# Kernel tuning notes

Measured on AMD Instinct MI355X. Metric: run time of the kernel, lower is better.

Reference implementation:

```python
import jax, jax.numpy as jnp
import numpy as np

N = 50000
E = 1600000
IN_F = 512
OUT_F = 128
NEG_SLOPE = 0.01   # nn.LeakyReLU() default
TEMPERATURE = 0.5


def setup_inputs() -> dict:
    key = jax.random.key(0)
    k1, k2, k3, k4 = jax.random.split(key, 4)
    h = jax.random.normal(k1, (N, IN_F), dtype=jnp.float32)
    # xavier_uniform with gain=1.414
    limW = 1.414 * np.sqrt(6.0 / (IN_F + OUT_F))
    W = jax.random.uniform(k2, (IN_F, OUT_F), minval=-limW, maxval=limW, dtype=jnp.float32)
    lima = 1.414 * np.sqrt(6.0 / (2 * OUT_F + 1))
    a = jax.random.uniform(k3, (2 * OUT_F, 1), minval=-lima, maxval=lima, dtype=jnp.float32)
    edge_index = jax.random.randint(k4, (2, E), 0, N, dtype=jnp.int64)
    return {"h": h, "W": W, "a": a, "edge_index": edge_index}


def reference(h, W, a, edge_index):
    # Inference: F.dropout(training=False) is identity.
    Wh = h @ W                                   # [N, F_out]
    src = edge_index[0]                          # row indices -> softmax segments
    dst = edge_index[1]
    # cat([Wh[src], Wh[dst]]) @ a == (Wh @ a1)[src] + (Wh @ a2)[dst]
    a1 = a[:OUT_F, 0]
    a2 = a[OUT_F:, 0]
    s1 = Wh @ a1                                 # [N]
    s2 = Wh @ a2                                 # [N]
    e = s1[src] + s2[dst]                        # [E]
    e = jnp.where(e >= 0, e, NEG_SLOPE * e)      # LeakyReLU
    logits = e / TEMPERATURE
    # sparse softmax over dim=1 (per source-node row segments)
    seg_max = jax.ops.segment_max(logits, src, num_segments=N)  # [N]
    ex = jnp.exp(logits - seg_max[src])          # [E]
    denom = jax.ops.segment_sum(ex, src, num_segments=N)        # [N]
    att = ex / denom[src]                        # [E]
    # sparse-dense matmul: h_prime[i] = sum_j att(i,j) * Wh[j]
    h_prime = jax.ops.segment_sum(att[:, None] * Wh[dst], src, num_segments=N)  # [N, F_out]
    return jax.nn.relu(h_prime)                  # concat=True path
```

## Files before the change

kernel.cpp:

```cpp
#include <hip/hip_runtime.h>
#include <cstdint>
#include <cstddef>

#define N_NODES 50000
#define N_EDGES 1600000
#define IN_FEAT 512
#define OUT_FEAT 128
#define NEG_SLOPE 0.01f
#define INV_TEMP 2.0f
#define PAD_DEG 128

#define BUCKETS 400
#define BNODES 125
#define BCAP 5000
#define A_BLOCKS 500
#define A_EPC (N_EDGES / A_BLOCKS)
#define A_G4 (A_EPC / 4)

#define CONV_BLOCKS ((IN_FEAT * OUT_FEAT) / 256)
#define GEMM_BLOCKS ((N_NODES + 127) / 128)

typedef __attribute__((ext_vector_type(8))) short short8;
typedef __attribute__((ext_vector_type(4))) float f32x4;

#define GLOBAL_AS __attribute__((address_space(1)))
#define LDS_AS __attribute__((address_space(3)))

__device__ inline unsigned short f2bf(float x) {
    unsigned int u = __float_as_uint(x);
    unsigned int r = (u + 0x7fffu + ((u >> 16) & 1u)) >> 16;
    return (unsigned short)r;
}
__device__ inline float bf2f(unsigned short b) {
    return __uint_as_float(((unsigned int)b) << 16);
}


__global__ __launch_bounds__(256) void convw_kernel(const float* __restrict__ W,
                                                    unsigned short* __restrict__ Wt,
                                                    int* __restrict__ bucket_cursor) {
    int tid = blockIdx.x * 256 + threadIdx.x;
    if (tid < BUCKETS) bucket_cursor[tid] = 0;
    if (tid < IN_FEAT * OUT_FEAT) {
        int n = tid >> 9;
        int k = tid & 511;
        Wt[tid] = f2bf(W[k * OUT_FEAT + n]);
    }
}


__global__ __launch_bounds__(512) void gemm_binA_kernel(const float* __restrict__ h,
                                                        const unsigned short* __restrict__ Wt,
                                                        const float* __restrict__ a_vec,
                                                        unsigned short* __restrict__ Whb,
                                                        float* __restrict__ s1,
                                                        float* __restrict__ s2,
                                                        const int* __restrict__ src,
                                                        const int* __restrict__ dst,
                                                        int* __restrict__ bucket_cursor,
                                                        int* __restrict__ binned) {
    __shared__ unsigned short lB[3][8 * 2 * 64 * 8];

    if (blockIdx.x >= GEMM_BLOCKS) {
        int* cntL = (int*)&lB[0][0];
        int* baseL = cntL + BUCKETS;
        int t = threadIdx.x;
        for (int i = t; i < BUCKETS; i += 512) cntL[i] = 0;
        __syncthreads();
        size_t ebase = (size_t)(blockIdx.x - GEMM_BLOCKS) * A_EPC;

        for (int g = t; g < A_G4; g += 512) {
            int4 s4 = *(const int4*)(src + ebase + (size_t)g * 4);
#pragma unroll
            for (int j = 0; j < 4; ++j) {
                int s = (&s4.x)[j];
                atomicAdd(&cntL[s / BNODES], 1);
            }
        }
        __syncthreads();
        for (int i = t; i < BUCKETS; i += 512) {
            int c = cntL[i];
            baseL[i] = c ? atomicAdd(&bucket_cursor[i], c) : 0;
            cntL[i] = 0;
        }
        __syncthreads();
        for (int g = t; g < A_G4; g += 512) {
            int4 s4 = *(const int4*)(src + ebase + (size_t)g * 4);
            int4 d4 = *(const int4*)(dst + ebase + (size_t)g * 4);
#pragma unroll
            for (int j = 0; j < 4; ++j) {
                int s = (&s4.x)[j];
                int b = s / BNODES;
                int sl = s - b * BNODES;
                int pos = atomicAdd(&cntL[b], 1);
                int slot = baseL[b] + pos;
                if (slot < BCAP)
                    binned[(size_t)b * BCAP + slot] = (sl << 16) | (&d4.x)[j];
            }
        }
        return;
    }

    int bid = blockIdx.x;
    int t = threadIdx.x;
    int w = t >> 6;
    int L = t & 63;
    int m0 = bid * 128;

    int arow = m0 + w * 16 + (L & 15);
    int arow_c = arow < N_NODES ? arow : N_NODES - 1;
    int kq = (L >> 4) * 8;
    const float* arp = h + (size_t)arow_c * IN_FEAT + kq;

    f32x4 acc[8];
#pragma unroll
    for (int i = 0; i < 8; ++i) acc[i] = (f32x4){0.f, 0.f, 0.f, 0.f};

    auto stageB = [&](int slot, int k0) {
#pragma unroll
        for (int ksub = 0; ksub < 2; ++ksub) {
            const GLOBAL_AS unsigned short* g =
                (const GLOBAL_AS unsigned short*)(Wt + (size_t)(w * 16 + (L & 15)) * IN_FEAT +
                                                  (k0 + ksub * 32 + kq));
            LDS_AS unsigned short* lp = (LDS_AS unsigned short*)(&lB[slot][(w * 2 + ksub) * 512]);
            __builtin_amdgcn_global_load_lds((const GLOBAL_AS void*)g, (LDS_AS void*)lp, 16, 0, 0);
        }
    };
    auto loadA = [&](int step, float4 out[4]) {
        const float* p = arp + step * 64;
        out[0] = *(const float4*)(p);
        out[1] = *(const float4*)(p + 4);
        out[2] = *(const float4*)(p + 32);
        out[3] = *(const float4*)(p + 36);
    };
    auto convA = [&](const float4 a[4], short8& f0, short8& f1) {
        short8 v;
        v[0] = (short)f2bf(a[0].x); v[1] = (short)f2bf(a[0].y);
        v[2] = (short)f2bf(a[0].z); v[3] = (short)f2bf(a[0].w);
        v[4] = (short)f2bf(a[1].x); v[5] = (short)f2bf(a[1].y);
        v[6] = (short)f2bf(a[1].z); v[7] = (short)f2bf(a[1].w);
        f0 = v;
        v[0] = (short)f2bf(a[2].x); v[1] = (short)f2bf(a[2].y);
        v[2] = (short)f2bf(a[2].z); v[3] = (short)f2bf(a[2].w);
        v[4] = (short)f2bf(a[3].x); v[5] = (short)f2bf(a[3].y);
        v[6] = (short)f2bf(a[3].z); v[7] = (short)f2bf(a[3].w);
        f1 = v;
    };

    float4 avA[4], avB[4], avC[4];
#pragma unroll
    for (int q = 0; q < 4; ++q) avC[q] = make_float4(0.f, 0.f, 0.f, 0.f);

    stageB(0, 0);
    asm volatile("" ::: "memory");
    stageB(1, 64);
    loadA(0, avA);
    loadA(1, avB);
    asm volatile("s_waitcnt vmcnt(10)" ::: "memory");
    __builtin_amdgcn_s_barrier();

#pragma unroll
    for (int it = 0; it < 8; ++it) {
        if (it < 6) {
            stageB((it + 2) % 3, (it + 2) * 64);
            loadA(it + 2, avC);
        }

        short8 af0, af1;
        convA(avA, af0, af1);

        const int buf = it % 3;
#pragma unroll
        for (int nb = 0; nb < 8; ++nb) {
            short8 bf = *(const short8*)(&lB[buf][((nb * 2 + 0) * 64 + L) * 8]);
            acc[nb] = __builtin_amdgcn_mfma_f32_16x16x32_bf16(af0, bf, acc[nb], 0, 0, 0);
        }
#pragma unroll
        for (int nb = 0; nb < 8; ++nb) {
            short8 bf = *(const short8*)(&lB[buf][((nb * 2 + 1) * 64 + L) * 8]);
            acc[nb] = __builtin_amdgcn_mfma_f32_16x16x32_bf16(af1, bf, acc[nb], 0, 0, 0);
        }

#pragma unroll
        for (int q = 0; q < 4; ++q) { avA[q] = avB[q]; avB[q] = avC[q]; }

        if (it < 6) {
            asm volatile("s_waitcnt vmcnt(6)" ::: "memory");
            __builtin_amdgcn_s_barrier();
        } else if (it == 6) {
            asm volatile("s_waitcnt vmcnt(0)" ::: "memory");
            __builtin_amdgcn_s_barrier();
        }
    }

    int col0 = L & 15;
    int rbase = m0 + w * 16 + (L >> 4) * 4;

    float a1c[8], a2c[8];
#pragma unroll
    for (int nb = 0; nb < 8; ++nb) {
        a1c[nb] = a_vec[nb * 16 + col0];
        a2c[nb] = a_vec[128 + nb * 16 + col0];
    }

#pragma unroll
    for (int r = 0; r < 4; ++r) {
        int row = rbase + r;
        bool ok = row < N_NODES;
        float p1 = 0.f, p2 = 0.f;
        if (ok) {
            unsigned short* orow = Whb + (size_t)row * OUT_FEAT;
#pragma unroll
            for (int nb = 0; nb < 8; ++nb) {
                float v = acc[nb][r];
                orow[nb * 16 + col0] = f2bf(v);
                p1 = fmaf(v, a1c[nb], p1);
                p2 = fmaf(v, a2c[nb], p2);
            }
        }
#pragma unroll
        for (int off = 8; off > 0; off >>= 1) {
            p1 += __shfl_xor(p1, off, 64);
            p2 += __shfl_xor(p2, off, 64);
        }
        if (ok && col0 == 0) {
            s1[row] = p1;
            s2[row] = p2;
        }
    }
}


__global__ __launch_bounds__(256) void binB_kernel(const int* __restrict__ bucket_cursor,
                                                   const int* __restrict__ binned,
                                                   int* __restrict__ cnt,
                                                   int* __restrict__ csr) {
    __shared__ int cL[BNODES];
    int b = blockIdx.x;
    int t = threadIdx.x;
    if (t < BNODES) cL[t] = 0;
    __syncthreads();
    int m = min(bucket_cursor[b], BCAP);
    const int* bp = binned + (size_t)b * BCAP;
    int n0 = b * BNODES;
    for (int i = t; i < m; i += 256) {
        int p = bp[i];
        int sl = p >> 16;
        int d = p & 0xFFFF;
        int pos = atomicAdd(&cL[sl], 1);
        if (pos < PAD_DEG) csr[(size_t)(n0 + sl) * PAD_DEG + pos] = d;
    }
    __syncthreads();
    if (t < BNODES) cnt[n0 + t] = min(cL[t], PAD_DEG);
}


__global__ __launch_bounds__(256) void node_kernel(const unsigned short* __restrict__ Whb,
                                                   const float* __restrict__ s1,
                                                   const float* __restrict__ s2,
                                                   const int* __restrict__ cnt,
                                                   const int* __restrict__ csr,
                                                   float* __restrict__ out) {
    int lane = threadIdx.x & 63;
    int w = threadIdx.x >> 6;
    int n = blockIdx.x * 4 + w;
    if (n >= N_NODES) return;
    int deg = cnt[n];
    size_t start = (size_t)n * PAD_DEG;
    int g = lane >> 4;
    int fo = lane & 15;

    float accv[8];
#pragma unroll
    for (int f = 0; f < 8; ++f) accv[f] = 0.f;
    float inv = 0.f;

    if (deg > 0) {
        float s1n = s1[n];
        int d0 = 0, d1 = 0;
        float ex0 = 0.f, ex1 = 0.f;
        if (lane < deg) {
            d0 = csr[start + lane];
            float ev = s1n + s2[d0];
            ev = ev >= 0.f ? ev : NEG_SLOPE * ev;
            ex0 = __expf(ev * INV_TEMP);
        }
        if (lane + 64 < deg) {
            d1 = csr[start + lane + 64];
            float ev = s1n + s2[d1];
            ev = ev >= 0.f ? ev : NEG_SLOPE * ev;
            ex1 = __expf(ev * INV_TEMP);
        }
        float denom = ex0 + ex1;
#pragma unroll
        for (int off = 32; off > 0; off >>= 1) denom += __shfl_xor(denom, off, 64);
        inv = 1.0f / denom;

#pragma unroll 2
        for (int jj = 0; jj < deg; jj += 8) {
            int e0 = jj + g;
            int e1 = jj + 4 + g;
            bool hi0 = jj >= 64;
            bool hi1 = (jj + 4) >= 64;
            float p0 = __shfl(hi0 ? ex1 : ex0, e0 & 63, 64);
            int dd0 = __shfl(hi0 ? d1 : d0, e0 & 63, 64);
            float p1 = __shfl(hi1 ? ex1 : ex0, e1 & 63, 64);
            int dd1 = __shfl(hi1 ? d1 : d0, e1 & 63, 64);
            short8 row0 = *(const short8*)(Whb + (size_t)dd0 * OUT_FEAT + fo * 8);
            short8 row1 = *(const short8*)(Whb + (size_t)dd1 * OUT_FEAT + fo * 8);
#pragma unroll
            for (int f = 0; f < 8; ++f)
                accv[f] = fmaf(p0, bf2f((unsigned short)row0[f]), accv[f]);
#pragma unroll
            for (int f = 0; f < 8; ++f)
                accv[f] = fmaf(p1, bf2f((unsigned short)row1[f]), accv[f]);
        }
#pragma unroll
        for (int f = 0; f < 8; ++f) {
            accv[f] += __shfl_xor(accv[f], 16, 64);
            accv[f] += __shfl_xor(accv[f], 32, 64);
        }
    }

    if (g == 0) {
        float* orow = out + (size_t)n * OUT_FEAT + fo * 8;
        float4 o0, o1;
        o0.x = fmaxf(accv[0] * inv, 0.f); o0.y = fmaxf(accv[1] * inv, 0.f);
        o0.z = fmaxf(accv[2] * inv, 0.f); o0.w = fmaxf(accv[3] * inv, 0.f);
        o1.x = fmaxf(accv[4] * inv, 0.f); o1.y = fmaxf(accv[5] * inv, 0.f);
        o1.z = fmaxf(accv[6] * inv, 0.f); o1.w = fmaxf(accv[7] * inv, 0.f);
        *(float4*)(orow) = o0;
        *(float4*)(orow + 4) = o1;
    }
}


extern "C" void kernel_launch(void* const* d_in, const int* in_sizes, int n_in,
                              void* d_out, int out_size, void* d_ws, size_t ws_size,
                              hipStream_t stream) {
    const float* h = (const float*)d_in[0];
    const float* W = (const float*)d_in[1];
    const float* a = (const float*)d_in[2];
    const int* edge = (const int*)d_in[3];
    const int* src = edge;
    const int* dst = edge + N_EDGES;
    float* out = (float*)d_out;

    char* ws = (char*)d_ws;
    size_t off = 0;
    auto alloc = [&](size_t bytes) -> void* {
        void* p = ws + off;
        off = (off + bytes + 255) & ~(size_t)255;
        return p;
    };
    unsigned short* Whb = (unsigned short*)alloc((size_t)N_NODES * OUT_FEAT * sizeof(unsigned short));
    float* s1 = (float*)alloc((size_t)N_NODES * sizeof(float));
    float* s2 = (float*)alloc((size_t)N_NODES * sizeof(float));
    int* cnt = (int*)alloc((size_t)N_NODES * sizeof(int));
    int* csr = (int*)alloc((size_t)N_NODES * PAD_DEG * sizeof(int));
    unsigned short* Wt = (unsigned short*)alloc((size_t)IN_FEAT * OUT_FEAT * sizeof(unsigned short));
    int* bucket_cursor = (int*)alloc((size_t)BUCKETS * sizeof(int));
    int* binned = (int*)alloc((size_t)BUCKETS * BCAP * sizeof(int));

    convw_kernel<<<CONV_BLOCKS, 256, 0, stream>>>(W, Wt, bucket_cursor);
    gemm_binA_kernel<<<GEMM_BLOCKS + A_BLOCKS, 512, 0, stream>>>(h, Wt, a, Whb, s1, s2,
                                                                 src, dst, bucket_cursor, binned);
    binB_kernel<<<BUCKETS, 256, 0, stream>>>(bucket_cursor, binned, cnt, csr);
    node_kernel<<<(N_NODES + 3) / 4, 256, 0, stream>>>(Whb, s1, s2, cnt, csr, out);
}
```

Measured before the change: 244.6 us.

## Fuse bucket-to-CSR binning into node aggregation kernel using shared-memory CSR

Merges the binB and node kernels into one launch per bucket: each 512-thread block builds its 125-node padded CSR in shared memory as 16-bit indices, then its 8 waves loop over those nodes to compute softmax and aggregation. This removes the global CSR and count arrays and their write-then-read round trip, plus one kernel launch. In exchange, only 400 blocks of 512 threads run the bandwidth-heavy gather phase, with about 32 KB of LDS per block, so fewer waves may be in flight to hide gather latency.

```diff
diff --git a/kernel.cpp b/kernel.cpp
--- a/kernel.cpp
+++ b/kernel.cpp
@@ -231,106 +231,103 @@
 }
 
 
-__global__ __launch_bounds__(256) void binB_kernel(const int* __restrict__ bucket_cursor,
-                                                   const int* __restrict__ binned,
-                                                   int* __restrict__ cnt,
-                                                   int* __restrict__ csr) {
+__global__ __launch_bounds__(512) void binB_node_kernel(const unsigned short* __restrict__ Whb,
+                                                        const float* __restrict__ s1,
+                                                        const float* __restrict__ s2,
+                                                        const int* __restrict__ bucket_cursor,
+                                                        const int* __restrict__ binned,
+                                                        float* __restrict__ out) {
     __shared__ int cL[BNODES];
+    __shared__ unsigned short csrL[BNODES * PAD_DEG];
     int b = blockIdx.x;
     int t = threadIdx.x;
+    int n0 = b * BNODES;
+
     if (t < BNODES) cL[t] = 0;
     __syncthreads();
     int m = min(bucket_cursor[b], BCAP);
     const int* bp = binned + (size_t)b * BCAP;
-    int n0 = b * BNODES;
-    for (int i = t; i < m; i += 256) {
+    for (int i = t; i < m; i += 512) {
         int p = bp[i];
         int sl = p >> 16;
         int d = p & 0xFFFF;
         int pos = atomicAdd(&cL[sl], 1);
-        if (pos < PAD_DEG) csr[(size_t)(n0 + sl) * PAD_DEG + pos] = d;
+        if (pos < PAD_DEG) csrL[sl * PAD_DEG + pos] = (unsigned short)d;
     }
     __syncthreads();
-    if (t < BNODES) cnt[n0 + t] = min(cL[t], PAD_DEG);
-}
-
-
-__global__ __launch_bounds__(256) void node_kernel(const unsigned short* __restrict__ Whb,
-                                                   const float* __restrict__ s1,
-                                                   const float* __restrict__ s2,
-                                                   const int* __restrict__ cnt,
-                                                   const int* __restrict__ csr,
-                                                   float* __restrict__ out) {
-    int lane = threadIdx.x & 63;
-    int w = threadIdx.x >> 6;
-    int n = blockIdx.x * 4 + w;
-    if (n >= N_NODES) return;
-    int deg = cnt[n];
-    size_t start = (size_t)n * PAD_DEG;
+
+    int lane = t & 63;
+    int w = t >> 6;
     int g = lane >> 4;
     int fo = lane & 15;
 
-    float accv[8];
-#pragma unroll
-    for (int f = 0; f < 8; ++f) accv[f] = 0.f;
-    float inv = 0.f;
-
-    if (deg > 0) {
-        float s1n = s1[n];
-        int d0 = 0, d1 = 0;
-        float ex0 = 0.f, ex1 = 0.f;
-        if (lane < deg) {
-            d0 = csr[start + lane];
-            float ev = s1n + s2[d0];
-            ev = ev >= 0.f ? ev : NEG_SLOPE * ev;
-            ex0 = __expf(ev * INV_TEMP);
-        }
-        if (lane + 64 < deg) {
-            d1 = csr[start + lane + 64];
-            float ev = s1n + s2[d1];
-            ev = ev >= 0.f ? ev : NEG_SLOPE * ev;
-            ex1 = __expf(ev * INV_TEMP);
-        }
-        float denom = ex0 + ex1;
-#pragma unroll
-        for (int off = 32; off > 0; off >>= 1) denom += __shfl_xor(denom, off, 64);
-        inv = 1.0f / denom;
+    for (int sl = w; sl < BNODES; sl += 8) {
+        int n = n0 + sl;
+        int deg = min(cL[sl], PAD_DEG);
+        const unsigned short* crow = &csrL[sl * PAD_DEG];
+
+        float accv[8];
+#pragma unroll
+        for (int f = 0; f < 8; ++f) accv[f] = 0.f;
+        float inv = 0.f;
+
+        if (deg > 0) {
+            float s1n = s1[n];
+            int d0 = 0, d1 = 0;
+            float ex0 = 0.f, ex1 = 0.f;
+            if (lane < deg) {
+                d0 = crow[lane];
+                float ev = s1n + s2[d0];
+                ev = ev >= 0.f ? ev : NEG_SLOPE * ev;
+                ex0 = __expf(ev * INV_TEMP);
+            }
+            if (lane + 64 < deg) {
+                d1 = crow[lane + 64];
+                float ev = s1n + s2[d1];
+                ev = ev >= 0.f ? ev : NEG_SLOPE * ev;
+                ex1 = __expf(ev * INV_TEMP);
+            }
+            float denom = ex0 + ex1;
+#pragma unroll
+            for (int off = 32; off > 0; off >>= 1) denom += __shfl_xor(denom, off, 64);
+            inv = 1.0f / denom;
 
 #pragma unroll 2
-        for (int jj = 0; jj < deg; jj += 8) {
-            int e0 = jj + g;
-            int e1 = jj + 4 + g;
-            bool hi0 = jj >= 64;
-            bool hi1 = (jj + 4) >= 64;
-            float p0 = __shfl(hi0 ? ex1 : ex0, e0 & 63, 64);
-            int dd0 = __shfl(hi0 ? d1 : d0, e0 & 63, 64);
-            float p1 = __shfl(hi1 ? ex1 : ex0, e1 & 63, 64);
-            int dd1 = __shfl(hi1 ? d1 : d0, e1 & 63, 64);
-            short8 row0 = *(const short8*)(Whb + (size_t)dd0 * OUT_FEAT + fo * 8);
-            short8 row1 = *(const short8*)(Whb + (size_t)dd1 * OUT_FEAT + fo * 8);
-#pragma unroll
-            for (int f = 0; f < 8; ++f)
-                accv[f] = fmaf(p0, bf2f((unsigned short)row0[f]), accv[f]);
-#pragma unroll
-            for (int f = 0; f < 8; ++f)
-                accv[f] = fmaf(p1, bf2f((unsigned short)row1[f]), accv[f]);
-        }
-#pragma unroll
-        for (int f = 0; f < 8; ++f) {
-            accv[f] += __shfl_xor(accv[f], 16, 64);
-            accv[f] += __shfl_xor(accv[f], 32, 64);
-        }
-    }
-
-    if (g == 0) {
-        float* orow = out + (size_t)n * OUT_FEAT + fo * 8;
-        float4 o0, o1;
-        o0.x = fmaxf(accv[0] * inv, 0.f); o0.y = fmaxf(accv[1] * inv, 0.f);
-        o0.z = fmaxf(accv[2] * inv, 0.f); o0.w = fmaxf(accv[3] * inv, 0.f);
-        o1.x = fmaxf(accv[4] * inv, 0.f); o1.y = fmaxf(accv[5] * inv, 0.f);
-        o1.z = fmaxf(accv[6] * inv, 0.f); o1.w = fmaxf(accv[7] * inv, 0.f);
-        *(float4*)(orow) = o0;
-        *(float4*)(orow + 4) = o1;
+            for (int jj = 0; jj < deg; jj += 8) {
+                int e0 = jj + g;
+                int e1 = jj + 4 + g;
+                bool hi0 = jj >= 64;
+                bool hi1 = (jj + 4) >= 64;
+                float p0 = __shfl(hi0 ? ex1 : ex0, e0 & 63, 64);
+                int dd0 = __shfl(hi0 ? d1 : d0, e0 & 63, 64);
+                float p1 = __shfl(hi1 ? ex1 : ex0, e1 & 63, 64);
+                int dd1 = __shfl(hi1 ? d1 : d0, e1 & 63, 64);
+                short8 row0 = *(const short8*)(Whb + (size_t)dd0 * OUT_FEAT + fo * 8);
+                short8 row1 = *(const short8*)(Whb + (size_t)dd1 * OUT_FEAT + fo * 8);
+#pragma unroll
+                for (int f = 0; f < 8; ++f)
+                    accv[f] = fmaf(p0, bf2f((unsigned short)row0[f]), accv[f]);
+#pragma unroll
+                for (int f = 0; f < 8; ++f)
+                    accv[f] = fmaf(p1, bf2f((unsigned short)row1[f]), accv[f]);
+            }
+#pragma unroll
+            for (int f = 0; f < 8; ++f) {
+                accv[f] += __shfl_xor(accv[f], 16, 64);
+                accv[f] += __shfl_xor(accv[f], 32, 64);
+            }
+        }
+
+        if (g == 0) {
+            float* orow = out + (size_t)n * OUT_FEAT + fo * 8;
+            float4 o0, o1;
+            o0.x = fmaxf(accv[0] * inv, 0.f); o0.y = fmaxf(accv[1] * inv, 0.f);
+            o0.z = fmaxf(accv[2] * inv, 0.f); o0.w = fmaxf(accv[3] * inv, 0.f);
+            o1.x = fmaxf(accv[4] * inv, 0.f); o1.y = fmaxf(accv[5] * inv, 0.f);
+            o1.z = fmaxf(accv[6] * inv, 0.f); o1.w = fmaxf(accv[7] * inv, 0.f);
+            *(float4*)(orow) = o0;
+            *(float4*)(orow + 4) = o1;
+        }
     }
 }
 
@@ -356,8 +353,6 @@
     unsigned short* Whb = (unsigned short*)alloc((size_t)N_NODES * OUT_FEAT * sizeof(unsigned short));
     float* s1 = (float*)alloc((size_t)N_NODES * sizeof(float));
     float* s2 = (float*)alloc((size_t)N_NODES * sizeof(float));
-    int* cnt = (int*)alloc((size_t)N_NODES * sizeof(int));
-    int* csr = (int*)alloc((size_t)N_NODES * PAD_DEG * sizeof(int));
     unsigned short* Wt = (unsigned short*)alloc((size_t)IN_FEAT * OUT_FEAT * sizeof(unsigned short));
     int* bucket_cursor = (int*)alloc((size_t)BUCKETS * sizeof(int));
     int* binned = (int*)alloc((size_t)BUCKETS * BCAP * sizeof(int));
@@ -365,6 +360,5 @@
     convw_kernel<<<CONV_BLOCKS, 256, 0, stream>>>(W, Wt, bucket_cursor);
     gemm_binA_kernel<<<GEMM_BLOCKS + A_BLOCKS, 512, 0, stream>>>(h, Wt, a, Whb, s1, s2,
                                                                  src, dst, bucket_cursor, binned);
-    binB_kernel<<<BUCKETS, 256, 0, stream>>>(bucket_cursor, binned, cnt, csr);
-    node_kernel<<<(N_NODES + 3) / 4, 256, 0, stream>>>(Whb, s1, s2, cnt, csr, out);
-}
+    binB_node_kernel<<<BUCKETS, 512, 0, stream>>>(Whb, s1, s2, bucket_cursor, binned, out);
+}
```

After: 241.4 us. Within noise of the previous version (-1.3%).
